# Kernel tuning notes

Hardware: AMD Instinct MI355X
Metric: run time of the kernel (lower is better)

## Reference

```python
import jax, jax.numpy as jnp
import numpy as np

N = 500_000      # total nodes
B = 4096         # number of graphs (batch.max()+1)
E = 512          # emb_dim (kdim/vdim)
D = 512          # output_dim
H = 8            # num_heads
DH = D // H      # head dim


def setup_inputs() -> dict:
    key = jax.random.key(0)
    ks = jax.random.split(key, 12)
    graph_emb = jax.random.normal(ks[0], (N, E), dtype=jnp.float32)
    batch = jnp.sort(jax.random.randint(ks[1], (N,), 0, B)).astype(jnp.int64)
    s = 0.02
    return {
        "graph_emb": graph_emb,
        "batch": batch,
        "qry": jax.random.normal(ks[2], (D,), dtype=jnp.float32),
        "Wq": jax.random.normal(ks[3], (D, D), dtype=jnp.float32) * s,
        "bq": jnp.zeros((D,), dtype=jnp.float32),
        "Wk": jax.random.normal(ks[4], (D, E), dtype=jnp.float32) * s,
        "bk": jnp.zeros((D,), dtype=jnp.float32),
        "Wv": jax.random.normal(ks[5], (D, E), dtype=jnp.float32) * s,
        "bv": jnp.zeros((D,), dtype=jnp.float32),
        "Wo": jax.random.normal(ks[6], (D, D), dtype=jnp.float32) * s,
        "bo": jnp.zeros((D,), dtype=jnp.float32),
    }


def reference(graph_emb, batch, qry, Wq, bq, Wk, bk, Wv, bv, Wo, bo):
    # Single learned query, shared across all graphs (torch repeats it).
    # q projection + torch MHA scaling by 1/sqrt(head_dim)
    q = (qry @ Wq.T + bq) / jnp.sqrt(jnp.asarray(DH, graph_emb.dtype))  # [D]
    q = q.reshape(H, DH)

    # per-node key/value projections
    k = (graph_emb @ Wk.T + bk).reshape(N, H, DH)  # [N,H,DH]
    v = (graph_emb @ Wv.T + bv).reshape(N, H, DH)  # [N,H,DH]

    # per-node, per-head attention logits against the shared query
    scores = jnp.einsum('nhd,hd->nh', k, q)  # [N,H]

    # segment-wise (per-graph) stable softmax; identical to padded softmax
    # with key_padding_mask since padded keys are fully masked out.
    smax = jax.ops.segment_max(scores, batch, num_segments=B,
                               indices_are_sorted=True)  # [B,H]
    w = jnp.exp(scores - smax[batch])                     # [N,H]
    denom = jax.ops.segment_sum(w, batch, num_segments=B,
                                indices_are_sorted=True)  # [B,H]
    num = jax.ops.segment_sum(w[:, :, None] * v, batch, num_segments=B,
                              indices_are_sorted=True)    # [B,H,DH]
    attn = num / denom[:, :, None]                        # [B,H,DH]

    out = attn.reshape(B, D) @ Wo.T + bo                  # [B,D]
    return out
```

## Files before the change

kernel.cpp:

```cpp
#include <hip/hip_runtime.h>

#define LOG2E 1.4426950408889634f

#define WK_OFF   ((size_t)0)
#define KB_OFF   ((size_t)16384)
#define Q2_OFF   ((size_t)16416)
#define SEG_OFF  ((size_t)18464)
#define S_OFF    ((size_t)34880)
#define ATTN_OFF ((size_t)33589312)
#define WS_NEEDED (ATTN_OFF + (size_t)4096*512*2)

__device__ __forceinline__ float readlane_f(float v, int l) {
  return __int_as_float(__builtin_amdgcn_readlane(__float_as_int(v), l));
}

__device__ __forceinline__ unsigned short f2bf(float x) {
  unsigned u = __float_as_uint(x);
  unsigned r = (u + 0x7fffu + ((u >> 16) & 1u)) >> 16;
  return (unsigned short)r;
}

__global__ __launch_bounds__(256) void k_q2(const float* __restrict__ qry,
                                            const float* __restrict__ Wq,
                                            const float* __restrict__ bq,
                                            float* __restrict__ q2) {
  int d = blockIdx.x * 256 + threadIdx.x;
  const float4* q4 = (const float4*)qry;
  const float4* w4 = (const float4*)(Wq + (size_t)d * 512);
  float acc = 0.f;
  #pragma unroll 4
  for (int j = 0; j < 128; ++j) {
    float4 a = q4[j], b = w4[j];
    acc += a.x * b.x + a.y * b.y + a.z * b.z + a.w * b.w;
  }
  q2[d] = (acc + bq[d]) * (0.125f * LOG2E);
}

__global__ __launch_bounds__(256) void k_wk(const float* __restrict__ Wk,
                                            const float* __restrict__ bk,
                                            const float* __restrict__ q2,
                                            float* __restrict__ wk,
                                            float* __restrict__ kb) {
  if (blockIdx.x == 16) {
    int h = threadIdx.x;
    if (h < 8) {
      float acc = 0.f;
      for (int dd = 0; dd < 64; ++dd) acc += q2[h * 64 + dd] * bk[h * 64 + dd];
      kb[h] = acc;
    }
    return;
  }
  int id = blockIdx.x * 256 + threadIdx.x;
  int h = id >> 9, e = id & 511;
  float acc = 0.f;
  #pragma unroll 4
  for (int dd = 0; dd < 64; ++dd)
    acc += q2[h * 64 + dd] * Wk[(size_t)(h * 64 + dd) * 512 + e];
  wk[id] = acc;
}

__global__ __launch_bounds__(256) void k_seg(const void* __restrict__ batch, int n,
                                             int* __restrict__ seg) {
  int b = blockIdx.x * 256 + threadIdx.x;
  if (b > 4096) return;
  const int* b32 = (const int*)batch;
  const long long* b64 = (const long long*)batch;
  bool is64 = (b32[n - 1] == 0);
  int lo = 0, hi = n;
  while (lo < hi) {
    int mid = (lo + hi) >> 1;
    long long v = is64 ? b64[mid] : (long long)b32[mid];
    if (v < (long long)b) lo = mid + 1; else hi = mid;
  }
  seg[b] = lo;
}

__global__ __launch_bounds__(256, 2) void k_main(const float* __restrict__ emb,
                                                 const int* __restrict__ seg,
                                                 const float* __restrict__ wk,
                                                 const float* __restrict__ kb,
                                                 unsigned short* __restrict__ S_ws) {
  __shared__ float sm[8232];
  const int tid = threadIdx.x;
  const int lane = tid & 63, wave = tid >> 6;
  const int b = blockIdx.x;
  const int s = seg[b], e2 = seg[b + 1];

  float4 wka[8], wkb[8];
  #pragma unroll
  for (int h = 0; h < 8; ++h) {
    wka[h] = *(const float4*)(wk + h * 512 + 4 * lane);
    wkb[h] = *(const float4*)(wk + h * 512 + 256 + 4 * lane);
  }
  const float kbl = kb[lane & 7];

  float4 Sa[8], Sb[8];
  #pragma unroll
  for (int h = 0; h < 8; ++h) {
    Sa[h] = make_float4(0.f, 0.f, 0.f, 0.f);
    Sb[h] = make_float4(0.f, 0.f, 0.f, 0.f);
  }
  float dn = 0.f;

  const float4* emb4 = (const float4*)emb;
  const int pw = wave * 832 + lane * 13;
  const int pr = wave * 832 + (lane & 56) * 13 + (lane & 7);

  int i = s + wave;
  if (i < e2) {
    size_t off = (size_t)i * 128 + lane;
    float4 a0 = emb4[off], a1 = emb4[off + 64];
    while (true) {
      int nx = i + 4;
      bool more = nx < e2;
      float4 b0, b1;
      if (more) {
        size_t o2 = (size_t)nx * 128 + lane;
        b0 = emb4[o2];
        b1 = emb4[o2 + 64];
      }
      float p[8];
      #pragma unroll
      for (int h = 0; h < 8; ++h) {
        float4 wa = wka[h], wb = wkb[h];
        p[h] = a0.x * wa.x + a0.y * wa.y + a0.z * wa.z + a0.w * wa.w +
               a1.x * wb.x + a1.y * wb.y + a1.z * wb.z + a1.w * wb.w;
      }
      #pragma unroll
      for (int h = 0; h < 8; ++h) sm[pw + h] = p[h];
      float hs = 0.f;
      #pragma unroll
      for (int j = 0; j < 8; ++j) hs += sm[pr + j * 13];
      hs += __shfl_xor(hs, 8);
      hs += __shfl_xor(hs, 16);
      hs += __shfl_xor(hs, 32);
      float w_own = exp2f(hs + kbl);
      dn += w_own;
      #pragma unroll
      for (int h = 0; h < 8; ++h) {
        float wh = readlane_f(w_own, h);
        Sa[h].x += wh * a0.x; Sa[h].y += wh * a0.y; Sa[h].z += wh * a0.z; Sa[h].w += wh * a0.w;
        Sb[h].x += wh * a1.x; Sb[h].y += wh * a1.y; Sb[h].z += wh * a1.z; Sb[h].w += wh * a1.w;
      }
      if (!more) break;
      i = nx; a0 = b0; a1 = b1;
    }
  }
  __syncthreads();

  if (lane < 8) sm[8192 + wave * 8 + lane] = dn;
  __syncthreads();
  if (tid < 8) {
    float d = sm[8192 + tid] + sm[8200 + tid] + sm[8208 + tid] + sm[8216 + tid];
    sm[8224 + tid] = (d > 0.f) ? 1.f / d : 0.f;
  }
  __syncthreads();

  #pragma unroll
  for (int h = 0; h < 8; ++h)
    *(float4*)&sm[wave * 2048 + h * 256 + 4 * lane] = Sa[h];
  __syncthreads();
  #pragma unroll
  for (int h = 0; h < 8; ++h) {
    float v = (sm[h * 256 + tid] + sm[2048 + h * 256 + tid] +
               sm[4096 + h * 256 + tid] + sm[6144 + h * 256 + tid]) * sm[8224 + h];
    S_ws[((size_t)h * 4096 + b) * 512 + tid] = f2bf(v);
  }
  __syncthreads();
  #pragma unroll
  for (int h = 0; h < 8; ++h)
    *(float4*)&sm[wave * 2048 + h * 256 + 4 * lane] = Sb[h];
  __syncthreads();
  #pragma unroll
  for (int h = 0; h < 8; ++h) {
    float v = (sm[h * 256 + tid] + sm[2048 + h * 256 + tid] +
               sm[4096 + h * 256 + tid] + sm[6144 + h * 256 + tid]) * sm[8224 + h];
    S_ws[((size_t)h * 4096 + b) * 512 + 256 + tid] = f2bf(v);
  }
}

template <bool C_BF16>
__global__ __launch_bounds__(256) void k_gemm(const unsigned short* __restrict__ A,
                                              size_t a_cb_stride,
                                              const float* __restrict__ W,
                                              const float* __restrict__ bias,
                                              void* __restrict__ Cv) {
  __shared__ float At[32][72];
  __shared__ float Wt[32][72];
  const int t = threadIdx.x;
  const int rt = blockIdx.x, cb = blockIdx.y;
  const int tm = t >> 4, tn = t & 15;
  const int r = t >> 2, c0 = (t & 3) * 8;
  const unsigned short* Ab = A + (size_t)cb * a_cb_stride + (size_t)(rt * 64 + r) * 512 + c0;
  const float* Wb = W + (size_t)(cb * 64 + r) * 512 + c0;
  float acc[4][4] = {};

  for (int kc = 0; kc < 512; kc += 32) {
    uint4 ar = *(const uint4*)(Ab + kc);
    float4 w0 = *(const float4*)(Wb + kc);
    float4 w1 = *(const float4*)(Wb + kc + 4);
    __syncthreads();
    At[c0 + 0][r] = __uint_as_float(ar.x << 16);
    At[c0 + 1][r] = __uint_as_float(ar.x & 0xffff0000u);
    At[c0 + 2][r] = __uint_as_float(ar.y << 16);
    At[c0 + 3][r] = __uint_as_float(ar.y & 0xffff0000u);
    At[c0 + 4][r] = __uint_as_float(ar.z << 16);
    At[c0 + 5][r] = __uint_as_float(ar.z & 0xffff0000u);
    At[c0 + 6][r] = __uint_as_float(ar.w << 16);
    At[c0 + 7][r] = __uint_as_float(ar.w & 0xffff0000u);
    Wt[c0 + 0][r] = w0.x; Wt[c0 + 1][r] = w0.y; Wt[c0 + 2][r] = w0.z; Wt[c0 + 3][r] = w0.w;
    Wt[c0 + 4][r] = w1.x; Wt[c0 + 5][r] = w1.y; Wt[c0 + 6][r] = w1.z; Wt[c0 + 7][r] = w1.w;
    __syncthreads();
    #pragma unroll
    for (int kk = 0; kk < 32; ++kk) {
      const float4 av = *(const float4*)&At[kk][tm * 4];
      const float4 wv = *(const float4*)&Wt[kk][tn * 4];
      acc[0][0] += av.x * wv.x; acc[0][1] += av.x * wv.y; acc[0][2] += av.x * wv.z; acc[0][3] += av.x * wv.w;
      acc[1][0] += av.y * wv.x; acc[1][1] += av.y * wv.y; acc[1][2] += av.y * wv.z; acc[1][3] += av.y * wv.w;
      acc[2][0] += av.z * wv.x; acc[2][1] += av.z * wv.y; acc[2][2] += av.z * wv.z; acc[2][3] += av.z * wv.w;
      acc[3][0] += av.w * wv.x; acc[3][1] += av.w * wv.y; acc[3][2] += av.w * wv.z; acc[3][3] += av.w * wv.w;
    }
  }

  const float4 bb = *(const float4*)(bias + cb * 64 + tn * 4);
  #pragma unroll
  for (int i2 = 0; i2 < 4; ++i2) {
    float x0 = acc[i2][0] + bb.x;
    float x1 = acc[i2][1] + bb.y;
    float x2 = acc[i2][2] + bb.z;
    float x3 = acc[i2][3] + bb.w;
    size_t row = (size_t)(rt * 64 + tm * 4 + i2);
    size_t col = (size_t)(cb * 64 + tn * 4);
    if (C_BF16) {
      unsigned int lo = (unsigned int)f2bf(x0) | ((unsigned int)f2bf(x1) << 16);
      unsigned int hi = (unsigned int)f2bf(x2) | ((unsigned int)f2bf(x3) << 16);
      *(uint2*)((unsigned short*)Cv + row * 512 + col) = make_uint2(lo, hi);
    } else {
      *(float4*)((float*)Cv + row * 512 + col) = make_float4(x0, x1, x2, x3);
    }
  }
}

extern "C" void kernel_launch(void* const* d_in, const int* in_sizes, int n_in,
                              void* d_out, int out_size, void* d_ws, size_t ws_size,
                              hipStream_t stream) {
  const float* emb  = (const float*)d_in[0];
  const void*  batch = d_in[1];
  const float* qry  = (const float*)d_in[2];
  const float* Wq   = (const float*)d_in[3];
  const float* bq   = (const float*)d_in[4];
  const float* Wk   = (const float*)d_in[5];
  const float* bk   = (const float*)d_in[6];
  const float* Wv   = (const float*)d_in[7];
  const float* bv   = (const float*)d_in[8];
  const float* Wo   = (const float*)d_in[9];
  const float* bo   = (const float*)d_in[10];
  const int N = in_sizes[1];

  if (ws_size < WS_NEEDED) return;

  char* ws = (char*)d_ws;
  float* q2     = (float*)(ws + Q2_OFF);
  float* wk_eff = (float*)(ws + WK_OFF);
  float* kbias  = (float*)(ws + KB_OFF);
  int*   seg    = (int*)(ws + SEG_OFF);
  unsigned short* S_ws = (unsigned short*)(ws + S_OFF);
  unsigned short* attn = (unsigned short*)(ws + ATTN_OFF);

  k_q2 <<<2, 256, 0, stream>>>(qry, Wq, bq, q2);
  k_wk <<<17, 256, 0, stream>>>(Wk, bk, q2, wk_eff, kbias);
  k_seg<<<17, 256, 0, stream>>>(batch, N, seg);
  k_main<<<4096, 256, 0, stream>>>(emb, seg, wk_eff, kbias, S_ws);
  dim3 g(64, 8);
  k_gemm<true ><<<g, 256, 0, stream>>>(S_ws, (size_t)4096 * 512, Wv, bv, attn);
  k_gemm<false><<<g, 256, 0, stream>>>(attn, 0, Wo, bo, d_out);
}
```

Baseline: 365.3 us.

## Use bf16 MFMA GEMMs with split weights, fuse prep kernels, unroll main loop

The two trailing scalar-FMA GEMMs become bf16 MFMA GEMMs. The fp32 Wv and Wo weights are split into hi/lo bf16 pairs in a new prep kernel so some weight precision is kept. The q2, segment and weight-split setup work is merged into one launch to cut launch overhead. The main streaming kernel now handles two nodes per wave iteration for more memory-level parallelism, at the cost of more register pressure. The GEMMs load operands straight from global memory without LDS staging, and their per-element epilogue stores are uncoalesced.

```diff
diff --git a/kernel.cpp b/kernel.cpp
--- a/kernel.cpp
+++ b/kernel.cpp
@@ -8,7 +8,14 @@
 #define SEG_OFF  ((size_t)18464)
 #define S_OFF    ((size_t)34880)
 #define ATTN_OFF ((size_t)33589312)
-#define WS_NEEDED (ATTN_OFF + (size_t)4096*512*2)
+#define WVHI_OFF ((size_t)37783616)
+#define WVLO_OFF ((size_t)38307904)
+#define WOHI_OFF ((size_t)38832192)
+#define WOLO_OFF ((size_t)39356480)
+#define WS_NEEDED ((size_t)39880768)
+
+typedef __bf16 bf16x8 __attribute__((ext_vector_type(8)));
+typedef float f32x4 __attribute__((ext_vector_type(4)));
 
 __device__ __forceinline__ float readlane_f(float v, int l) {
   return __int_as_float(__builtin_amdgcn_readlane(__float_as_int(v), l));
@@ -20,20 +27,53 @@
   return (unsigned short)r;
 }
 
-__global__ __launch_bounds__(256) void k_q2(const float* __restrict__ qry,
-                                            const float* __restrict__ Wq,
-                                            const float* __restrict__ bq,
-                                            float* __restrict__ q2) {
-  int d = blockIdx.x * 256 + threadIdx.x;
-  const float4* q4 = (const float4*)qry;
-  const float4* w4 = (const float4*)(Wq + (size_t)d * 512);
-  float acc = 0.f;
-  #pragma unroll 4
-  for (int j = 0; j < 128; ++j) {
-    float4 a = q4[j], b = w4[j];
-    acc += a.x * b.x + a.y * b.y + a.z * b.z + a.w * b.w;
-  }
-  q2[d] = (acc + bq[d]) * (0.125f * LOG2E);
+__device__ __forceinline__ float bf2f(unsigned short h) {
+  return __uint_as_float((unsigned)h << 16);
+}
+
+__global__ __launch_bounds__(256) void k_prep(
+    const float* __restrict__ Wv, const float* __restrict__ Wo,
+    unsigned short* __restrict__ wvhi, unsigned short* __restrict__ wvlo,
+    unsigned short* __restrict__ wohi, unsigned short* __restrict__ wolo,
+    const void* __restrict__ batch, int n, int* __restrict__ seg,
+    const float* __restrict__ qry, const float* __restrict__ Wq,
+    const float* __restrict__ bq, float* __restrict__ q2) {
+  int bx = blockIdx.x;
+  if (bx < 1024) {
+    int i = bx * 256 + threadIdx.x;
+    float v = Wv[i];
+    unsigned short h = f2bf(v);
+    wvhi[i] = h;
+    wvlo[i] = f2bf(v - bf2f(h));
+    float o = Wo[i];
+    unsigned short h2 = f2bf(o);
+    wohi[i] = h2;
+    wolo[i] = f2bf(o - bf2f(h2));
+  } else if (bx < 1041) {
+    int b = (bx - 1024) * 256 + threadIdx.x;
+    if (b > 4096) return;
+    const int* b32 = (const int*)batch;
+    const long long* b64 = (const long long*)batch;
+    bool is64 = (b32[n - 1] == 0);
+    int lo = 0, hi = n;
+    while (lo < hi) {
+      int mid = (lo + hi) >> 1;
+      long long v = is64 ? b64[mid] : (long long)b32[mid];
+      if (v < (long long)b) lo = mid + 1; else hi = mid;
+    }
+    seg[b] = lo;
+  } else {
+    int d = (bx - 1041) * 256 + threadIdx.x;
+    const float4* q4 = (const float4*)qry;
+    const float4* w4 = (const float4*)(Wq + (size_t)d * 512);
+    float acc = 0.f;
+    #pragma unroll 4
+    for (int j = 0; j < 128; ++j) {
+      float4 a = q4[j], b = w4[j];
+      acc += a.x * b.x + a.y * b.y + a.z * b.z + a.w * b.w;
+    }
+    q2[d] = (acc + bq[d]) * (0.125f * LOG2E);
+  }
 }
 
 __global__ __launch_bounds__(256) void k_wk(const float* __restrict__ Wk,
@@ -59,22 +99,6 @@
   wk[id] = acc;
 }
 
-__global__ __launch_bounds__(256) void k_seg(const void* __restrict__ batch, int n,
-                                             int* __restrict__ seg) {
-  int b = blockIdx.x * 256 + threadIdx.x;
-  if (b > 4096) return;
-  const int* b32 = (const int*)batch;
-  const long long* b64 = (const long long*)batch;
-  bool is64 = (b32[n - 1] == 0);
-  int lo = 0, hi = n;
-  while (lo < hi) {
-    int mid = (lo + hi) >> 1;
-    long long v = is64 ? b64[mid] : (long long)b32[mid];
-    if (v < (long long)b) lo = mid + 1; else hi = mid;
-  }
-  seg[b] = lo;
-}
-
 __global__ __launch_bounds__(256, 2) void k_main(const float* __restrict__ emb,
                                                  const int* __restrict__ seg,
                                                  const float* __restrict__ wk,
@@ -103,47 +127,70 @@
   float dn = 0.f;
 
   const float4* emb4 = (const float4*)emb;
-  const int pw = wave * 832 + lane * 13;
-  const int pr = wave * 832 + (lane & 56) * 13 + (lane & 7);
-
-  int i = s + wave;
+  const int pw = wave * 1088 + lane * 17;
+  const int pr = wave * 1088 + (lane & 56) * 17 + (lane & 7);
+
+  int i = s + wave * 2;
   if (i < e2) {
-    size_t off = (size_t)i * 128 + lane;
-    float4 a0 = emb4[off], a1 = emb4[off + 64];
+    size_t o = (size_t)i * 128 + lane;
+    float4 a0 = emb4[o], a1 = emb4[o + 64];
+    bool v1 = (i + 1) < e2;
+    float4 a2, a3;
+    if (v1) { a2 = emb4[o + 128]; a3 = emb4[o + 192]; }
     while (true) {
-      int nx = i + 4;
-      bool more = nx < e2;
-      float4 b0, b1;
-      if (more) {
+      int nx = i + 8;
+      bool m0 = nx < e2;
+      bool m1 = (nx + 1) < e2;
+      float4 b0, b1, b2, b3;
+      if (m0) {
         size_t o2 = (size_t)nx * 128 + lane;
-        b0 = emb4[o2];
-        b1 = emb4[o2 + 64];
-      }
-      float p[8];
+        b0 = emb4[o2]; b1 = emb4[o2 + 64];
+        if (m1) { b2 = emb4[o2 + 128]; b3 = emb4[o2 + 192]; }
+      }
       #pragma unroll
       for (int h = 0; h < 8; ++h) {
         float4 wa = wka[h], wb = wkb[h];
-        p[h] = a0.x * wa.x + a0.y * wa.y + a0.z * wa.z + a0.w * wa.w +
-               a1.x * wb.x + a1.y * wb.y + a1.z * wb.z + a1.w * wb.w;
-      }
+        sm[pw + h] = a0.x * wa.x + a0.y * wa.y + a0.z * wa.z + a0.w * wa.w +
+                     a1.x * wb.x + a1.y * wb.y + a1.z * wb.z + a1.w * wb.w;
+        if (v1)
+          sm[pw + 8 + h] = a2.x * wa.x + a2.y * wa.y + a2.z * wa.z + a2.w * wa.w +
+                           a3.x * wb.x + a3.y * wb.y + a3.z * wb.z + a3.w * wb.w;
+      }
+      float hs0 = 0.f;
       #pragma unroll
-      for (int h = 0; h < 8; ++h) sm[pw + h] = p[h];
-      float hs = 0.f;
-      #pragma unroll
-      for (int j = 0; j < 8; ++j) hs += sm[pr + j * 13];
-      hs += __shfl_xor(hs, 8);
-      hs += __shfl_xor(hs, 16);
-      hs += __shfl_xor(hs, 32);
-      float w_own = exp2f(hs + kbl);
-      dn += w_own;
+      for (int j = 0; j < 8; ++j) hs0 += sm[pr + j * 17];
+      hs0 += __shfl_xor(hs0, 8);
+      hs0 += __shfl_xor(hs0, 16);
+      hs0 += __shfl_xor(hs0, 32);
+      float w0 = exp2f(hs0 + kbl);
+      dn += w0;
       #pragma unroll
       for (int h = 0; h < 8; ++h) {
-        float wh = readlane_f(w_own, h);
+        float wh = readlane_f(w0, h);
         Sa[h].x += wh * a0.x; Sa[h].y += wh * a0.y; Sa[h].z += wh * a0.z; Sa[h].w += wh * a0.w;
         Sb[h].x += wh * a1.x; Sb[h].y += wh * a1.y; Sb[h].z += wh * a1.z; Sb[h].w += wh * a1.w;
       }
-      if (!more) break;
-      i = nx; a0 = b0; a1 = b1;
+      if (v1) {
+        float hs1 = 0.f;
+        #pragma unroll
+        for (int j = 0; j < 8; ++j) hs1 += sm[pr + 8 + j * 17];
+        hs1 += __shfl_xor(hs1, 8);
+        hs1 += __shfl_xor(hs1, 16);
+        hs1 += __shfl_xor(hs1, 32);
+        float w1 = exp2f(hs1 + kbl);
+        dn += w1;
+        #pragma unroll
+        for (int h = 0; h < 8; ++h) {
+          float wh = readlane_f(w1, h);
+          Sa[h].x += wh * a2.x; Sa[h].y += wh * a2.y; Sa[h].z += wh * a2.z; Sa[h].w += wh * a2.w;
+          Sb[h].x += wh * a3.x; Sb[h].y += wh * a3.y; Sb[h].z += wh * a3.z; Sb[h].w += wh * a3.w;
+        }
+      }
+      if (!m0) break;
+      i = nx;
+      a0 = b0; a1 = b1;
+      v1 = m1;
+      if (m1) { a2 = b2; a3 = b3; }
     }
   }
   __syncthreads();
@@ -180,63 +227,59 @@
 }
 
 template <bool C_BF16>
-__global__ __launch_bounds__(256) void k_gemm(const unsigned short* __restrict__ A,
-                                              size_t a_cb_stride,
-                                              const float* __restrict__ W,
-                                              const float* __restrict__ bias,
-                                              void* __restrict__ Cv) {
-  __shared__ float At[32][72];
-  __shared__ float Wt[32][72];
+__global__ __launch_bounds__(256) void k_gemm_mfma(
+    const unsigned short* __restrict__ A, size_t a_cb_stride,
+    const unsigned short* __restrict__ Whi, const unsigned short* __restrict__ Wlo,
+    const float* __restrict__ bias, void* __restrict__ Cv) {
   const int t = threadIdx.x;
-  const int rt = blockIdx.x, cb = blockIdx.y;
-  const int tm = t >> 4, tn = t & 15;
-  const int r = t >> 2, c0 = (t & 3) * 8;
-  const unsigned short* Ab = A + (size_t)cb * a_cb_stride + (size_t)(rt * 64 + r) * 512 + c0;
-  const float* Wb = W + (size_t)(cb * 64 + r) * 512 + c0;
-  float acc[4][4] = {};
-
-  for (int kc = 0; kc < 512; kc += 32) {
-    uint4 ar = *(const uint4*)(Ab + kc);
-    float4 w0 = *(const float4*)(Wb + kc);
-    float4 w1 = *(const float4*)(Wb + kc + 4);
-    __syncthreads();
-    At[c0 + 0][r] = __uint_as_float(ar.x << 16);
-    At[c0 + 1][r] = __uint_as_float(ar.x & 0xffff0000u);
-    At[c0 + 2][r] = __uint_as_float(ar.y << 16);
-    At[c0 + 3][r] = __uint_as_float(ar.y & 0xffff0000u);
-    At[c0 + 4][r] = __uint_as_float(ar.z << 16);
-    At[c0 + 5][r] = __uint_as_float(ar.z & 0xffff0000u);
-    At[c0 + 6][r] = __uint_as_float(ar.w << 16);
-    At[c0 + 7][r] = __uint_as_float(ar.w & 0xffff0000u);
-    Wt[c0 + 0][r] = w0.x; Wt[c0 + 1][r] = w0.y; Wt[c0 + 2][r] = w0.z; Wt[c0 + 3][r] = w0.w;
-    Wt[c0 + 4][r] = w1.x; Wt[c0 + 5][r] = w1.y; Wt[c0 + 6][r] = w1.z; Wt[c0 + 7][r] = w1.w;
-    __syncthreads();
+  const int lane = t & 63, wvid = t >> 6;
+  const int wr = wvid >> 1, wc = wvid & 1;
+  const int row16 = lane & 15;
+  const int k8 = (lane >> 4) * 8;
+  const int mbase = blockIdx.x * 64 + wr * 32;
+  const int nbase = blockIdx.y * 64 + wc * 32;
+
+  const unsigned short* Ap = A + (size_t)blockIdx.y * a_cb_stride +
+                             (size_t)(mbase + row16) * 512 + k8;
+  const unsigned short* Wh = Whi + (size_t)(nbase + row16) * 512 + k8;
+  const unsigned short* Wl = Wlo + (size_t)(nbase + row16) * 512 + k8;
+
+  f32x4 acc[2][2] = {};
+
+  #pragma unroll 4
+  for (int kk = 0; kk < 512; kk += 32) {
+    bf16x8 a0 = *(const bf16x8*)(Ap + kk);
+    bf16x8 a1 = *(const bf16x8*)(Ap + 16 * 512 + kk);
+    bf16x8 h0 = *(const bf16x8*)(Wh + kk);
+    bf16x8 h1 = *(const bf16x8*)(Wh + 16 * 512 + kk);
+    bf16x8 l0 = *(const bf16x8*)(Wl + kk);
+    bf16x8 l1 = *(const bf16x8*)(Wl + 16 * 512 + kk);
+    acc[0][0] = __builtin_amdgcn_mfma_f32_16x16x32_bf16(a0, h0, acc[0][0], 0, 0, 0);
+    acc[0][1] = __builtin_amdgcn_mfma_f32_16x16x32_bf16(a0, h1, acc[0][1], 0, 0, 0);
+    acc[1][0] = __builtin_amdgcn_mfma_f32_16x16x32_bf16(a1, h0, acc[1][0], 0, 0, 0);
+    acc[1][1] = __builtin_amdgcn_mfma_f32_16x16x32_bf16(a1, h1, acc[1][1], 0, 0, 0);
+    acc[0][0] = __builtin_amdgcn_mfma_f32_16x16x32_bf16(a0, l0, acc[0][0], 0, 0, 0);
+    acc[0][1] = __builtin_amdgcn_mfma_f32_16x16x32_bf16(a0, l1, acc[0][1], 0, 0, 0);
+    acc[1][0] = __builtin_amdgcn_mfma_f32_16x16x32_bf16(a1, l0, acc[1][0], 0, 0, 0);
+    acc[1][1] = __builtin_amdgcn_mfma_f32_16x16x32_bf16(a1, l1, acc[1][1], 0, 0, 0);
+  }
+
+  const int r4 = (lane >> 4) * 4;
+  #pragma unroll
+  for (int c = 0; c < 2; ++c) {
+    const float bc = bias[nbase + c * 16 + row16];
     #pragma unroll
-    for (int kk = 0; kk < 32; ++kk) {
-      const float4 av = *(const float4*)&At[kk][tm * 4];
-      const float4 wv = *(const float4*)&Wt[kk][tn * 4];
-      acc[0][0] += av.x * wv.x; acc[0][1] += av.x * wv.y; acc[0][2] += av.x * wv.z; acc[0][3] += av.x * wv.w;
-      acc[1][0] += av.y * wv.x; acc[1][1] += av.y * wv.y; acc[1][2] += av.y * wv.z; acc[1][3] += av.y * wv.w;
-      acc[2][0] += av.z * wv.x; acc[2][1] += av.z * wv.y; acc[2][2] += av.z * wv.z; acc[2][3] += av.z * wv.w;
-      acc[3][0] += av.w * wv.x; acc[3][1] += av.w * wv.y; acc[3][2] += av.w * wv.z; acc[3][3] += av.w * wv.w;
-    }
-  }
-
-  const float4 bb = *(const float4*)(bias + cb * 64 + tn * 4);
-  #pragma unroll
-  for (int i2 = 0; i2 < 4; ++i2) {
-    float x0 = acc[i2][0] + bb.x;
-    float x1 = acc[i2][1] + bb.y;
-    float x2 = acc[i2][2] + bb.z;
-    float x3 = acc[i2][3] + bb.w;
-    size_t row = (size_t)(rt * 64 + tm * 4 + i2);
-    size_t col = (size_t)(cb * 64 + tn * 4);
-    if (C_BF16) {
-      unsigned int lo = (unsigned int)f2bf(x0) | ((unsigned int)f2bf(x1) << 16);
-      unsigned int hi = (unsigned int)f2bf(x2) | ((unsigned int)f2bf(x3) << 16);
-      *(uint2*)((unsigned short*)Cv + row * 512 + col) = make_uint2(lo, hi);
-    } else {
-      *(float4*)((float*)Cv + row * 512 + col) = make_float4(x0, x1, x2, x3);
+    for (int r = 0; r < 2; ++r) {
+      #pragma unroll
+      for (int j = 0; j < 4; ++j) {
+        float v = acc[r][c][j] + bc;
+        size_t row = (size_t)(mbase + r * 16 + r4 + j);
+        size_t col = (size_t)(nbase + c * 16 + row16);
+        if (C_BF16)
+          ((unsigned short*)Cv)[row * 512 + col] = f2bf(v);
+        else
+          ((float*)Cv)[row * 512 + col] = v;
+      }
     }
   }
 }
@@ -244,34 +287,38 @@
 extern "C" void kernel_launch(void* const* d_in, const int* in_sizes, int n_in,
                               void* d_out, int out_size, void* d_ws, size_t ws_size,
                               hipStream_t stream) {
-  const float* emb  = (const float*)d_in[0];
+  const float* emb   = (const float*)d_in[0];
   const void*  batch = d_in[1];
-  const float* qry  = (const float*)d_in[2];
-  const float* Wq   = (const float*)d_in[3];
-  const float* bq   = (const float*)d_in[4];
-  const float* Wk   = (const float*)d_in[5];
-  const float* bk   = (const float*)d_in[6];
-  const float* Wv   = (const float*)d_in[7];
-  const float* bv   = (const float*)d_in[8];
-  const float* Wo   = (const float*)d_in[9];
-  const float* bo   = (const float*)d_in[10];
+  const float* qry   = (const float*)d_in[2];
+  const float* Wq    = (const float*)d_in[3];
+  const float* bq    = (const float*)d_in[4];
+  const float* Wk    = (const float*)d_in[5];
+  const float* bk    = (const float*)d_in[6];
+  const float* Wv    = (const float*)d_in[7];
+  const float* bv    = (const float*)d_in[8];
+  const float* Wo    = (const float*)d_in[9];
+  const float* bo    = (const float*)d_in[10];
   const int N = in_sizes[1];
 
   if (ws_size < WS_NEEDED) return;
 
   char* ws = (char*)d_ws;
-  float* q2     = (float*)(ws + Q2_OFF);
   float* wk_eff = (float*)(ws + WK_OFF);
   float* kbias  = (float*)(ws + KB_OFF);
+  float* q2     = (float*)(ws + Q2_OFF);
   int*   seg    = (int*)(ws + SEG_OFF);
   unsigned short* S_ws = (unsigned short*)(ws + S_OFF);
   unsigned short* attn = (unsigned short*)(ws + ATTN_OFF);
-
-  k_q2 <<<2, 256, 0, stream>>>(qry, Wq, bq, q2);
-  k_wk <<<17, 256, 0, stream>>>(Wk, bk, q2, wk_eff, kbias);
-  k_seg<<<17, 256, 0, stream>>>(batch, N, seg);
+  unsigned short* wvhi = (unsigned short*)(ws + WVHI_OFF);
+  unsigned short* wvlo = (unsigned short*)(ws + WVLO_OFF);
+  unsigned short* wohi = (unsigned short*)(ws + WOHI_OFF);
+  unsigned short* wolo = (unsigned short*)(ws + WOLO_OFF);
+
+  k_prep<<<1043, 256, 0, stream>>>(Wv, Wo, wvhi, wvlo, wohi, wolo,
+                                   batch, N, seg, qry, Wq, bq, q2);
+  k_wk  <<<17, 256, 0, stream>>>(Wk, bk, q2, wk_eff, kbias);
   k_main<<<4096, 256, 0, stream>>>(emb, seg, wk_eff, kbias, S_ws);
   dim3 g(64, 8);
-  k_gemm<true ><<<g, 256, 0, stream>>>(S_ws, (size_t)4096 * 512, Wv, bv, attn);
-  k_gemm<false><<<g, 256, 0, stream>>>(attn, 0, Wo, bo, d_out);
-}
+  k_gemm_mfma<true ><<<g, 256, 0, stream>>>(S_ws, (size_t)4096 * 512, wvhi, wvlo, bv, attn);
+  k_gemm_mfma<false><<<g, 256, 0, stream>>>(attn, 0, wohi, wolo, bo, d_out);
+}
```

Result: no change. 364.8 us (-0.1%).
